# Performance work log

Measured on AMD Instinct MI355X. Metric: run time of the kernel, lower is better.

Reference implementation:

```python
import jax, jax.numpy as jnp
import numpy as np

FS = 512.0
N_PHA = 10
N_AMP = 10
FIR_LEN = 513  # odd, ~1 s at fs=512 -> resolves 2 Hz band edges
N_BINS = 18    # hard-coded in PAC.__init__
TEMP = 0.01    # ModulationIndex temperature (near-hard soft binning)
EPS = 1e-8


def _design_filters():
    # Windowed-sinc FIR bandpass, one kernel per band: h = lp(hi) - lp(lo), Hamming window.
    t = np.arange(FIR_LEN) - (FIR_LEN - 1) / 2.0
    win = np.hamming(FIR_LEN)
    def bp(lo, hi):
        lp = lambda fc: 2.0 * fc / FS * np.sinc(2.0 * fc / FS * t)
        return (lp(hi) - lp(lo)) * win
    pha_c = np.linspace(2.0, 20.0, N_PHA)
    amp_c = np.linspace(60.0, 160.0, N_AMP)
    bands = [(0.75 * c, 1.25 * c) for c in pha_c] + [(0.75 * c, 1.25 * c) for c in amp_c]
    return np.stack([bp(lo, hi) for lo, hi in bands]).astype(np.float32)  # (20, L)


def setup_inputs() -> dict:
    key = jax.random.key(0)
    x = jax.random.normal(key, (4, 16, 4096), dtype=jnp.float32)  # (B, C, T)
    filters = jnp.asarray(_design_filters())                      # (n_pha+n_amp, L)
    return {"x": x, "filters": filters}


def _analytic(sig):
    # FFT-based Hilbert analytic signal along last axis.
    T = sig.shape[-1]
    h = np.zeros(T, np.float32)
    h[0] = 1.0
    if T % 2 == 0:
        h[T // 2] = 1.0
        h[1:T // 2] = 2.0
    else:
        h[1:(T + 1) // 2] = 2.0
    return jnp.fft.ifft(jnp.fft.fft(sig, axis=-1) * jnp.asarray(h), axis=-1)


def reference(x, filters):
    B, C, T = x.shape
    L = filters.shape[-1]
    # Bandpass: (B*C, 1, T) x (n_bands, 1, L) -> (B*C, n_bands, T); symmetric kernels so corr == conv.
    xf = jax.lax.conv_general_dilated(
        x.reshape(-1, 1, T), filters[:, None, :],
        window_strides=(1,), padding=[(L // 2, L // 2)])
    xf = xf.reshape(B, C, -1, T)
    phase = jnp.angle(_analytic(xf[:, :, :N_PHA]))        # (B, C, P, T)
    amplitude = jnp.abs(_analytic(xf[:, :, N_PHA:]))      # (B, C, A, T)
    # Soft circular phase binning (temperature -> near one-hot).
    centers = jnp.asarray((-np.pi + 2.0 * np.pi * (np.arange(N_BINS) + 0.5) / N_BINS).astype(np.float32))
    d = jnp.mod(phase[..., None] - centers + np.pi, 2.0 * np.pi) - np.pi  # (B,C,P,T,K)
    w = jax.nn.softmax(-(d * d) / TEMP, axis=-1)
    # Mean amplitude per phase bin, per (pha, amp) band pair.
    amp_sum = jnp.einsum('bcptk,bcat->bcpak', w, amplitude)  # (B,C,P,A,K)
    cnt = w.sum(axis=-2)                                      # (B,C,P,K)
    mean_amp = amp_sum / (cnt[:, :, :, None, :] + EPS)
    p = mean_amp / (mean_amp.sum(-1, keepdims=True) + EPS)
    log_k = jnp.log(jnp.float32(N_BINS))
    mi = (log_k + (p * jnp.log(p + EPS)).sum(-1)) / log_k    # Tort MI, (B,C,P,A)
    return mi
```

## Files before the change

### kernel.cpp

```cpp
#include <hip/hip_runtime.h>
#include <math.h>

#define T_LEN 4096
#define FIR_L 513
#define N_PHA 10
#define N_AMP 10
#define N_BANDS 20
#define N_BINS 18
#define BC 64

typedef __attribute__((ext_vector_type(8))) short short8;
typedef __attribute__((ext_vector_type(4))) float f32x4;

#define ZA(i) (((i) << 1) + ((((i) >> 4)) << 1))

__device__ float2 twg_dev[1024];

static __device__ __forceinline__ unsigned short f2bf(float x) {
    unsigned u = __float_as_uint(x);
    unsigned r = u + 0x7FFFu + ((u >> 16) & 1u);
    return (unsigned short)(r >> 16);
}

static __device__ __forceinline__ float fast_atan2f(float y, float x) {
    const float ax = fabsf(x), ay = fabsf(y);
    const float mx = fmaxf(ax, ay), mn = fminf(ax, ay);
    const bool swap = ay > ax;
    const bool red  = mn > 0.4142135623730950f * mx;
    const float num = red ? (mn - mx) : mn;
    const float den = red ? (mn + mx) : mx;
    const float u  = num / den;
    const float z2 = u * u;
    float p = fmaf(8.05374449538e-2f, z2, -1.38776856032e-1f);
    p = fmaf(p, z2, 1.99777106478e-1f);
    p = fmaf(p, z2, -3.33329491539e-1f);
    float a = fmaf(p * z2, u, u);
    if (red)  a += 0.7853981633974483f;
    if (swap) a = 1.5707963267948966f - a;
    if (x < 0.0f) a = 3.14159265358979323f - a;
    return (y < 0.0f) ? -a : a;
}

static __device__ __forceinline__ void tw_derive(const float2* tw, int m1,
        float& c1, float& s1, float& c2, float& s2, float& c3, float& s3) {
    const float2 w1 = tw[m1];
    c1 = w1.x; s1 = w1.y;
    s2 = 2.0f * s1 * c1;
    c2 = fmaf(-2.0f * s1, s1, 1.0f);
    c3 = c1 * c2 - s1 * s2;
    s3 = s1 * c2 + c1 * s2;
}

static __device__ __forceinline__ float2 cmul_em(float2 u, float c, float s) {
    return make_float2(u.x * c + u.y * s, u.y * c - u.x * s);
}

static __device__ __forceinline__ void bf_fwd(float2& A, float2& B, float2& C, float2& D,
        float c1, float s1, float c2, float s2, float c3, float s3) {
    const float t0r = A.x + C.x, t0i = A.y + C.y;
    const float t1r = A.x - C.x, t1i = A.y - C.y;
    const float t2r = B.x + D.x, t2i = B.y + D.y;
    const float t3r = B.x - D.x, t3i = B.y - D.y;
    const float y0r = t0r + t2r,  y0i = t0i + t2i;
    const float u1r = t1r + t3i, u1i = t1i - t3r;
    const float u2r = t0r - t2r, u2i = t0i - t2i;
    const float u3r = t1r - t3i, u3i = t1i + t3r;
    A = make_float2(y0r, y0i);
    B = make_float2(u1r * c1 + u1i * s1, u1i * c1 - u1r * s1);
    C = make_float2(u2r * c2 + u2i * s2, u2i * c2 - u2r * s2);
    D = make_float2(u3r * c3 + u3i * s3, u3i * c3 - u3r * s3);
}

static __device__ __forceinline__ void bf_inv(float2& A, float2& B, float2& C, float2& D,
        float c1, float s1, float c2, float s2, float c3, float s3) {
    const float tbr = B.x * c1 - B.y * s1, tbi = B.y * c1 + B.x * s1;
    const float tcr = C.x * c2 - C.y * s2, tci = C.y * c2 + C.x * s2;
    const float tdr = D.x * c3 - D.y * s3, tdi = D.y * c3 + D.x * s3;
    const float ar = A.x, ai = A.y;
    A = make_float2(ar + tbr + tcr + tdr, ai + tbi + tci + tdi);
    B = make_float2(ar - tbi - tcr + tdi, ai + tbr - tci - tdr);
    C = make_float2(ar - tbr + tcr - tdr, ai - tbi + tci - tdi);
    D = make_float2(ar + tbi - tcr - tdi, ai - tbr - tci + tdr);
}

static __device__ __forceinline__ void fft_fwd_passes(float* z, const float2* tw,
                                                      int tid, int s0) {
    for (int s = s0; s < 6; s += 2) {
        const int hl = 10 - 2 * s;
        const int h  = 1 << hl;
        const int h4 = h >> 2;
        const int kk = tid & (h4 - 1);
        const int g  = tid >> (hl - 2);
        const int i0 = (g << (hl + 2)) + kk;
        float2 e[4][4];
#pragma unroll
        for (int j = 0; j < 4; ++j)
#pragma unroll
            for (int r = 0; r < 4; ++r)
                e[j][r] = *(const float2*)&z[ZA(i0 + j * h4 + r * h)];
#pragma unroll
        for (int j = 0; j < 4; ++j) {
            float c1, s1, c2, s2, c3, s3;
            tw_derive(tw, (kk + j * h4) << (2 * s), c1, s1, c2, s2, c3, s3);
            bf_fwd(e[j][0], e[j][1], e[j][2], e[j][3], c1, s1, c2, s2, c3, s3);
        }
        {
            float c1, s1, c2, s2, c3, s3;
            tw_derive(tw, kk << (2 * s + 2), c1, s1, c2, s2, c3, s3);
#pragma unroll
            for (int r = 0; r < 4; ++r)
                bf_fwd(e[0][r], e[1][r], e[2][r], e[3][r], c1, s1, c2, s2, c3, s3);
        }
#pragma unroll
        for (int j = 0; j < 4; ++j)
#pragma unroll
            for (int r = 0; r < 4; ++r)
                *(float2*)&z[ZA(i0 + j * h4 + r * h)] = e[j][r];
        __syncthreads();
    }
}

static __device__ __forceinline__ void fft_fwd_pass1_sparse(
        float* z, const float2* tw, int tid, float2 F, float2 Tl) {
    float c1, s1, c2, s2, c3, s3;
    tw_derive(tw, tid, c1, s1, c2, s2, c3, s3);
    float2 P[4];
    P[0] = F;
    P[1] = cmul_em(F, c1, s1);
    P[2] = cmul_em(F, c2, s2);
    P[3] = cmul_em(F, c3, s3);
    tw_derive(tw, tid + 768, c1, s1, c2, s2, c3, s3);
    const float2 iT  = make_float2(-Tl.y,  Tl.x);
    const float2 nT  = make_float2(-Tl.x, -Tl.y);
    const float2 niT = make_float2( Tl.y, -Tl.x);
    float2 Q[4];
    Q[0] = Tl;
    Q[1] = cmul_em(iT,  c1, s1);
    Q[2] = cmul_em(nT,  c2, s2);
    Q[3] = cmul_em(niT, c3, s3);
    tw_derive(tw, tid << 2, c1, s1, c2, s2, c3, s3);
#pragma unroll
    for (int r = 0; r < 4; ++r) {
        const int ib = tid + (r << 10);
        const float2 A = make_float2(P[r].x + Q[r].x, P[r].y + Q[r].y);
        const float2 B = cmul_em(make_float2(P[r].x - Q[r].y, P[r].y + Q[r].x), c1, s1);
        const float2 C = cmul_em(make_float2(P[r].x - Q[r].x, P[r].y - Q[r].y), c2, s2);
        const float2 D = cmul_em(make_float2(P[r].x + Q[r].y, P[r].y - Q[r].x), c3, s3);
        *(float2*)&z[ZA(ib)]        = A;
        *(float2*)&z[ZA(ib + 256)]  = B;
        *(float2*)&z[ZA(ib + 512)]  = C;
        *(float2*)&z[ZA(ib + 768)]  = D;
    }
}

static __device__ __forceinline__ void fft_inv6(float* z, const float2* tw, int tid) {
#pragma unroll
    for (int s = 0; s < 6; s += 2) {
        const int L  = 1 << (2 * s);
        const int k  = tid & (L - 1);
        const int g  = tid >> (2 * s);
        const int i0 = (g << (2 * s + 4)) + k;
        float2 e[4][4];
#pragma unroll
        for (int j = 0; j < 4; ++j)
#pragma unroll
            for (int r = 0; r < 4; ++r)
                e[j][r] = *(const float2*)&z[ZA(i0 + j * L + (r << (2 * s + 2)))];
        {
            float c1, s1, c2, s2, c3, s3;
            tw_derive(tw, k << (10 - 2 * s), c1, s1, c2, s2, c3, s3);
#pragma unroll
            for (int r = 0; r < 4; ++r)
                bf_inv(e[0][r], e[1][r], e[2][r], e[3][r], c1, s1, c2, s2, c3, s3);
        }
#pragma unroll
        for (int j = 0; j < 4; ++j) {
            float c1, s1, c2, s2, c3, s3;
            tw_derive(tw, (k + j * L) << (8 - 2 * s), c1, s1, c2, s2, c3, s3);
            bf_inv(e[j][0], e[j][1], e[j][2], e[j][3], c1, s1, c2, s2, c3, s3);
        }
#pragma unroll
        for (int j = 0; j < 4; ++j)
#pragma unroll
            for (int r = 0; r < 4; ++r)
                *(float2*)&z[ZA(i0 + j * L + (r << (2 * s + 2)))] = e[j][r];
        __syncthreads();
    }
}

__global__ __launch_bounds__(256) void spectral_pre(
    const float* __restrict__ x,
    const float* __restrict__ filt,
    float2* __restrict__ Xs,
    float2* __restrict__ Hs,
    float* __restrict__ corr)
{
    __shared__ __align__(16) float sm[11265];

    const int tid = threadIdx.x;
    const int b   = blockIdx.x;

    if (b == BC + N_BANDS) {
        for (int m = tid; m < 1024; m += 256) {
            float ang = (float)m * (6.283185307179586f / 4096.0f);
            float s, c;
            sincosf(ang, &s, &c);
            twg_dev[m] = make_float2(c, s);
        }
        return;
    }

    if (b > BC + N_BANDS) {
        const int cidx = b - (BC + N_BANDS + 1);
        const int bc   = cidx / N_BANDS;
        const int band = cidx % N_BANDS;
        float* xe = sm;
        float* fb = sm + 512;

        const float* xrow = x + bc * T_LEN;
        for (int i = tid; i < 512; i += 256)
            xe[i] = (i < 256) ? xrow[i] : xrow[3584 + i];
        for (int i = tid; i < FIR_L; i += 256)
            fb[i] = filt[band * FIR_L + i];
        __syncthreads();

        const int t = tid;
        float cf = 0.0f, ct = 0.0f;
        for (int l = 0; l <= 255 - t; ++l)
            cf = fmaf(fb[l], xe[256 + t + l], cf);
        for (int j = 0; j <= t; ++j)
            ct = fmaf(fb[512 - t + j], xe[j], ct);

        corr[((bc * N_BANDS + band) * 2 + 0) * 256 + t] = cf;
        corr[((bc * N_BANDS + band) * 2 + 1) * 256 + t] = ct;
        return;
    }

    float*  z   = sm;
    float2* twl = (float2*)(sm + 8704);
    float*  fb  = sm + 8704 + 2048;

    for (int m = tid; m < 1024; m += 256) {
        float ang = (float)m * (6.283185307179586f / 4096.0f);
        float s, c;
        sincosf(ang, &s, &c);
        twl[m] = make_float2(c, s);
    }

    if (b < BC) {
        const float* xrow = x + b * T_LEN;
        for (int i = tid; i < 4096; i += 256)
            *(float2*)&z[ZA(i)] = make_float2(xrow[i], 0.0f);
    } else {
        const int band = b - BC;
        for (int i = tid; i < FIR_L; i += 256) fb[i] = filt[band * FIR_L + i];
        __syncthreads();
        for (int i = tid; i < 4096; i += 256) {
            float hv = 0.0f;
            if (i < 257)        hv = fb[256 - i];
            else if (i >= 3840) hv = fb[4352 - i];
            *(float2*)&z[ZA(i)] = make_float2(hv, 0.0f);
        }
    }
    __syncthreads();

    fft_fwd_passes(z, twl, tid, 0);

    float2* dst = (b < BC) ? (Xs + b * 4096) : (Hs + (b - BC) * 4096);
    for (int i = tid; i < 4096; i += 256)
        dst[i] = *(const float2*)&z[ZA(i)];
}

__global__ __launch_bounds__(256, 4) void spectral_main_pre(
    const float* __restrict__ corr,
    const float2* __restrict__ Xs,
    const float2* __restrict__ Hs,
    float* __restrict__ pha,
    unsigned short* __restrict__ amp_bf)
{
    __shared__ __align__(16) float z[8704];

    const int tid  = threadIdx.x;
    const int bc   = blockIdx.x / N_BANDS;
    const int band = blockIdx.x % N_BANDS;
    const float2* tw = twg_dev;

    const float cf = corr[((bc * N_BANDS + band) * 2 + 0) * 256 + tid];
    const float ct = corr[((bc * N_BANDS + band) * 2 + 1) * 256 + tid];

    fft_fwd_pass1_sparse(z, tw, tid, make_float2(-cf, 0.0f), make_float2(-ct, 0.0f));
    __syncthreads();
    fft_fwd_passes(z, tw, tid, 2);

    const float2* Xrow = Xs + bc * 4096;
    const float2* Hrow = Hs + band * 4096;
#pragma unroll
    for (int k = 0; k < 8; ++k) {
        const int s = tid + (k << 8);
        const int i = ((s >> 1) << 2) | (s & 1);
        const float2 X = Xrow[i];
        const float2 H = Hrow[i];
        const float2 C = *(const float2*)&z[ZA(i)];
        const float pr = X.x * H.x - X.y * H.y + C.x;
        const float pi = X.x * H.y + X.y * H.x + C.y;
        const float mf = (i == 0) ? 1.0f : 2.0f;
        *(float2*)&z[ZA(i)] = make_float2(pr * mf, pi * mf);
    }
#pragma unroll
    for (int k = 0; k < 8; ++k) {
        const int s = tid + (k << 8);
        const int i = ((s >> 1) << 2) | 2 | (s & 1);
        if (i == 2) {
            const float2 X = Xrow[2];
            const float2 H = Hrow[2];
            const float2 C = *(const float2*)&z[ZA(2)];
            *(float2*)&z[ZA(2)] = make_float2(X.x * H.x - X.y * H.y + C.x,
                                              X.x * H.y + X.y * H.x + C.y);
        } else {
            *(float2*)&z[ZA(i)] = make_float2(0.0f, 0.0f);
        }
    }
    __syncthreads();

    fft_inv6(z, tw, tid);

    const float inv_n = 1.0f / 4096.0f;
    if (band < N_PHA) {
        float* dst = pha + (bc * N_PHA + band) * T_LEN;
        for (int i = tid; i < 4096; i += 256) {
            const float2 zz = *(const float2*)&z[ZA(i)];
            dst[i] = fast_atan2f(zz.y, zz.x);
        }
    } else {
        unsigned short* dst = amp_bf + (bc * N_AMP + (band - N_PHA)) * T_LEN;
        for (int i = tid; i < 4096; i += 256) {
            const float2 zz = *(const float2*)&z[ZA(i)];
            dst[i] = f2bf(sqrtf(zz.x * zz.x + zz.y * zz.y) * inv_n);
        }
    }
}

__global__ __launch_bounds__(256, 4) void spectral_main_inline(
    const float* __restrict__ x,
    const float* __restrict__ filt,
    const float2* __restrict__ Xs,
    const float2* __restrict__ Hs,
    float* __restrict__ pha,
    unsigned short* __restrict__ amp_bf)
{
    __shared__ float z[8704];
    __shared__ float xe[512];
    __shared__ float fb[FIR_L];

    const int tid  = threadIdx.x;
    const int bc   = blockIdx.x / N_BANDS;
    const int band = blockIdx.x % N_BANDS;
    const float2* tw = twg_dev;

    const float* xrow = x + bc * T_LEN;
    for (int i = tid; i < 512; i += 256)
        xe[i] = (i < 256) ? xrow[i] : xrow[3584 + i];
    for (int i = tid; i < FIR_L; i += 256) fb[i] = filt[band * FIR_L + i];
    __syncthreads();

    float cf = 0.0f, ct = 0.0f;
    for (int l = 0; l <= 255 - tid; ++l)
        cf = fmaf(fb[l], xe[256 + tid + l], cf);
    for (int j = 0; j <= tid; ++j)
        ct = fmaf(fb[512 - tid + j], xe[j], ct);

    fft_fwd_pass1_sparse(z, tw, tid, make_float2(-cf, 0.0f), make_float2(-ct, 0.0f));
    __syncthreads();
    fft_fwd_passes(z, tw, tid, 2);

    const float2* Xrow = Xs + bc * 4096;
    const float2* Hrow = Hs + band * 4096;
    for (int i = tid; i < 4096; i += 256) {
        const float2 X = Xrow[i];
        const float2 H = Hrow[i];
        const float2 C = *(const float2*)&z[ZA(i)];
        float pr = X.x * H.x - X.y * H.y + C.x;
        float pi = X.x * H.y + X.y * H.x + C.y;
        const int m4 = i & 3;
        const float mf = (i == 0 || i == 2) ? 1.0f : (m4 < 2 ? 2.0f : 0.0f);
        *(float2*)&z[ZA(i)] = make_float2(pr * mf, pi * mf);
    }
    __syncthreads();

    fft_inv6(z, tw, tid);

    const float inv_n = 1.0f / 4096.0f;
    if (band < N_PHA) {
        float* dst = pha + (bc * N_PHA + band) * T_LEN;
        for (int i = tid; i < 4096; i += 256) {
            const float2 zz = *(const float2*)&z[ZA(i)];
            dst[i] = fast_atan2f(zz.y, zz.x);
        }
    } else {
        unsigned short* dst = amp_bf + (bc * N_AMP + (band - N_PHA)) * T_LEN;
        for (int i = tid; i < 4096; i += 256) {
            const float2 zz = *(const float2*)&z[ZA(i)];
            dst[i] = f2bf(sqrtf(zz.x * zz.x + zz.y * zz.y) * inv_n);
        }
    }
}

__global__ __launch_bounds__(512) void bin_mi_mfma(
    const float* __restrict__ pha,
    const unsigned short* __restrict__ amp_bf,
    float* __restrict__ out)
{
    const int tid  = threadIdx.x;
    const int lane = tid & 63;
    const int wv   = tid >> 6;
    const int bc   = blockIdx.x / N_PHA;
    const int p    = blockIdx.x % N_PHA;

    __shared__ unsigned int wbufW[8][18 * 68];
    __shared__ float psum[8][11][N_BINS];
    __shared__ float asum[11][N_BINS];

    const float* phrow = pha + (bc * N_PHA + p) * T_LEN;
    const unsigned short* arow = amp_bf + bc * N_AMP * T_LEN;

    const float PI_F  = 3.14159274101257324f;
    const float INVD  = 2.8647889756541160f;
    const float DELTA = 0.34906585039886590f;
    const float C1    = 12.184696791468343f;
    const float C2    = 69.813170079773180f;

    const int m_ = lane & 15;
    const int q_ = lane >> 4;
    const int n_ = lane & 15;

    short8 zero8;
#pragma unroll
    for (int j = 0; j < 8; ++j) zero8[j] = 0;
    short8 ones8;
#pragma unroll
    for (int j = 0; j < 8; ++j) ones8[j] = (short)0x3F80;

    f32x4 acc0 = {0.f, 0.f, 0.f, 0.f};
    f32x4 acc1 = {0.f, 0.f, 0.f, 0.f};

    const int base_t = wv * 512;
    unsigned short* wh = (unsigned short*)&wbufW[wv][0];

    float2 pp[4];
#pragma unroll
    for (int c = 0; c < 4; ++c)
        pp[c] = *(const float2*)&phrow[base_t + c * 128 + lane * 2];

    for (int chunk = 0; chunk < 4; ++chunk) {
        const int cb = base_t + chunk * 128;

        short8 af[4];
#pragma unroll
        for (int s = 0; s < 4; ++s) {
            const int tA = cb + s * 32 + q_ * 8;
            if (m_ < N_AMP)       af[s] = *(const short8*)(arow + m_ * T_LEN + tA);
            else if (m_ == N_AMP) af[s] = ones8;
            else                  af[s] = zero8;
        }

#pragma unroll
        for (int k = 0; k < N_BINS; ++k)
            wbufW[wv][k * 68 + lane] = 0u;

#pragma unroll
        for (int h = 0; h < 2; ++h) {
            const float ph = h ? pp[chunk].y : pp[chunk].x;
            float u  = (ph + PI_F) * INVD;
            float jf = floorf(u);
            float d  = (u - jf - 0.5f) * DELTA;
            int j0 = (int)jf;
            if (j0 >= N_BINS) j0 -= N_BINS;
            const int jm = (j0 == 0) ? N_BINS - 1 : j0 - 1;
            const int jp = (j0 == N_BINS - 1) ? 0 : j0 + 1;
            const float em = expf(-C1 - C2 * d);
            const float ep = expf(-C1 + C2 * d);
            const float inv = 1.0f / (1.0f + em + ep);
            wh[(j0 * 68 + lane) * 2 + h] = f2bf(inv);
            wh[(jm * 68 + lane) * 2 + h] = f2bf(em * inv);
            wh[(jp * 68 + lane) * 2 + h] = f2bf(ep * inv);
        }
        __builtin_amdgcn_wave_barrier();

#pragma unroll
        for (int s = 0; s < 4; ++s) {
            const int woff = s * 16 + q_ * 4;
            short8 bfrag0 = *(const short8*)&wbufW[wv][n_ * 68 + woff];
            short8 bfrag1 = (n_ < 2)
                ? *(const short8*)&wbufW[wv][(16 + n_) * 68 + woff]
                : zero8;
            acc0 = __builtin_amdgcn_mfma_f32_16x16x32_bf16(af[s], bfrag0, acc0, 0, 0, 0);
            acc1 = __builtin_amdgcn_mfma_f32_16x16x32_bf16(af[s], bfrag1, acc1, 0, 0, 0);
        }
        __builtin_amdgcn_wave_barrier();
    }

#pragma unroll
    for (int r = 0; r < 4; ++r) {
        const int m = q_ * 4 + r;
        if (m < 11) {
            psum[wv][m][n_] = acc0[r];
            if (n_ < 2) psum[wv][m][16 + n_] = acc1[r];
        }
    }
    __syncthreads();

    if (tid < 11 * N_BINS) {
        const int m = tid / N_BINS;
        const int k = tid % N_BINS;
        float s = 0.0f;
#pragma unroll
        for (int w = 0; w < 8; ++w) s += psum[w][m][k];
        asum[m][k] = s;
    }
    __syncthreads();

    if (tid < N_AMP) {
        float ma[N_BINS];
        float msum = 0.0f;
#pragma unroll
        for (int k = 0; k < N_BINS; ++k) {
            float m = asum[tid][k] / (asum[10][k] + 1e-8f);
            ma[k] = m;
            msum += m;
        }
        const float inv = 1.0f / (msum + 1e-8f);
        float acc = 0.0f;
#pragma unroll
        for (int k = 0; k < N_BINS; ++k) {
            float pk = ma[k] * inv;
            acc = fmaf(pk, logf(pk + 1e-8f), acc);
        }
        const float logk = 2.89037175789124f;
        out[(bc * N_PHA + p) * N_AMP + tid] = (logk + acc) / logk;
    }
}

extern "C" void kernel_launch(void* const* d_in, const int* in_sizes, int n_in,
                              void* d_out, int out_size, void* d_ws, size_t ws_size,
                              hipStream_t stream) {
    const float* x    = (const float*)d_in[0];
    const float* filt = (const float*)d_in[1];
    float* out = (float*)d_out;

    float* pha = (float*)d_ws;
    unsigned short* amp_bf = (unsigned short*)(pha + BC * N_PHA * T_LEN);
    float2* Xs = (float2*)(amp_bf + BC * N_AMP * T_LEN);
    float2* Hs = Xs + BC * 4096;
    float* corr = (float*)(Hs + N_BANDS * 4096);

    const size_t need = (size_t)BC * N_PHA * T_LEN * 4
                      + (size_t)BC * N_AMP * T_LEN * 2
                      + (size_t)BC * 4096 * 8
                      + (size_t)N_BANDS * 4096 * 8
                      + (size_t)BC * N_BANDS * 2 * 256 * 4;
    const bool fits = (ws_size >= need);

    if (fits) {
        spectral_pre<<<BC + N_BANDS + 1 + BC * N_BANDS, 256, 0, stream>>>(x, filt, Xs, Hs, corr);
        spectral_main_pre<<<BC * N_BANDS, 256, 0, stream>>>(corr, Xs, Hs, pha, amp_bf);
    } else {
        spectral_pre<<<BC + N_BANDS + 1, 256, 0, stream>>>(x, filt, Xs, Hs, corr);
        spectral_main_inline<<<BC * N_BANDS, 256, 0, stream>>>(x, filt, Xs, Hs, pha, amp_bf);
    }
    bin_mi_mfma<<<BC * N_PHA, 512, 0, stream>>>(pha, amp_bf, out);
}
```

Baseline: 115.3 us.

## Fuse last forward FFT pass, spectral multiply and first inverse pass in registers

In the main spectral kernel, the final forward radix-16 pass, the Hilbert spectral multiply/mask and the first inverse radix-16 pass now run on the same 16 register-resident elements per thread. This drops two shared-memory round trips and barriers. The last inverse pass is also kept in registers, and phase and amplitude are written straight from them rather than re-read from LDS. FFT passes are split into fwd_pair/inv_pair helpers, with twiddle-free butterflies where the twiddles are trivial. The costs are higher register pressure and more complex indexing.

```diff
diff --git a/kernel.cpp b/kernel.cpp
--- a/kernel.cpp
+++ b/kernel.cpp
@@ -71,6 +71,17 @@
     D = make_float2(u3r * c3 + u3i * s3, u3i * c3 - u3r * s3);
 }
 
+static __device__ __forceinline__ void bf_fwd_nw(float2& A, float2& B, float2& C, float2& D) {
+    const float t0r = A.x + C.x, t0i = A.y + C.y;
+    const float t1r = A.x - C.x, t1i = A.y - C.y;
+    const float t2r = B.x + D.x, t2i = B.y + D.y;
+    const float t3r = B.x - D.x, t3i = B.y - D.y;
+    A = make_float2(t0r + t2r, t0i + t2i);
+    B = make_float2(t1r + t3i, t1i - t3r);
+    C = make_float2(t0r - t2r, t0i - t2i);
+    D = make_float2(t1r - t3i, t1i + t3r);
+}
+
 static __device__ __forceinline__ void bf_inv(float2& A, float2& B, float2& C, float2& D,
         float c1, float s1, float c2, float s2, float c3, float s3) {
     const float tbr = B.x * c1 - B.y * s1, tbi = B.y * c1 + B.x * s1;
@@ -83,41 +94,88 @@
     D = make_float2(ar + tbi - tcr - tdi, ai - tbr - tci + tdr);
 }
 
+static __device__ __forceinline__ void bf_inv_nw(float2& A, float2& B, float2& C, float2& D) {
+    const float tbr = B.x, tbi = B.y;
+    const float tcr = C.x, tci = C.y;
+    const float tdr = D.x, tdi = D.y;
+    const float ar = A.x, ai = A.y;
+    A = make_float2(ar + tbr + tcr + tdr, ai + tbi + tci + tdi);
+    B = make_float2(ar - tbi - tcr + tdi, ai + tbr - tci - tdr);
+    C = make_float2(ar - tbr + tcr - tdr, ai - tbi + tci - tdi);
+    D = make_float2(ar + tbi - tcr - tdi, ai - tbr - tci + tdr);
+}
+
+static __device__ __forceinline__ void fwd_pair(float* z, const float2* tw,
+                                                int tid, int s) {
+    const int hl = 10 - 2 * s;
+    const int h  = 1 << hl;
+    const int h4 = h >> 2;
+    const int kk = tid & (h4 - 1);
+    const int g  = tid >> (hl - 2);
+    const int i0 = (g << (hl + 2)) + kk;
+    float2 e[4][4];
+#pragma unroll
+    for (int j = 0; j < 4; ++j)
+#pragma unroll
+        for (int r = 0; r < 4; ++r)
+            e[j][r] = *(const float2*)&z[ZA(i0 + j * h4 + r * h)];
+#pragma unroll
+    for (int j = 0; j < 4; ++j) {
+        float c1, s1, c2, s2, c3, s3;
+        tw_derive(tw, (kk + j * h4) << (2 * s), c1, s1, c2, s2, c3, s3);
+        bf_fwd(e[j][0], e[j][1], e[j][2], e[j][3], c1, s1, c2, s2, c3, s3);
+    }
+    {
+        float c1, s1, c2, s2, c3, s3;
+        tw_derive(tw, kk << (2 * s + 2), c1, s1, c2, s2, c3, s3);
+#pragma unroll
+        for (int r = 0; r < 4; ++r)
+            bf_fwd(e[0][r], e[1][r], e[2][r], e[3][r], c1, s1, c2, s2, c3, s3);
+    }
+#pragma unroll
+    for (int j = 0; j < 4; ++j)
+#pragma unroll
+        for (int r = 0; r < 4; ++r)
+            *(float2*)&z[ZA(i0 + j * h4 + r * h)] = e[j][r];
+    __syncthreads();
+}
+
+static __device__ __forceinline__ void inv_pair(float* z, const float2* tw,
+                                                int tid, int s) {
+    const int L  = 1 << (2 * s);
+    const int k  = tid & (L - 1);
+    const int g  = tid >> (2 * s);
+    const int i0 = (g << (2 * s + 4)) + k;
+    float2 e[4][4];
+#pragma unroll
+    for (int j = 0; j < 4; ++j)
+#pragma unroll
+        for (int r = 0; r < 4; ++r)
+            e[j][r] = *(const float2*)&z[ZA(i0 + j * L + (r << (2 * s + 2)))];
+    {
+        float c1, s1, c2, s2, c3, s3;
+        tw_derive(tw, k << (10 - 2 * s), c1, s1, c2, s2, c3, s3);
+#pragma unroll
+        for (int r = 0; r < 4; ++r)
+            bf_inv(e[0][r], e[1][r], e[2][r], e[3][r], c1, s1, c2, s2, c3, s3);
+    }
+#pragma unroll
+    for (int j = 0; j < 4; ++j) {
+        float c1, s1, c2, s2, c3, s3;
+        tw_derive(tw, (k + j * L) << (8 - 2 * s), c1, s1, c2, s2, c3, s3);
+        bf_inv(e[j][0], e[j][1], e[j][2], e[j][3], c1, s1, c2, s2, c3, s3);
+    }
+#pragma unroll
+    for (int j = 0; j < 4; ++j)
+#pragma unroll
+        for (int r = 0; r < 4; ++r)
+            *(float2*)&z[ZA(i0 + j * L + (r << (2 * s + 2)))] = e[j][r];
+    __syncthreads();
+}
+
 static __device__ __forceinline__ void fft_fwd_passes(float* z, const float2* tw,
                                                       int tid, int s0) {
-    for (int s = s0; s < 6; s += 2) {
-        const int hl = 10 - 2 * s;
-        const int h  = 1 << hl;
-        const int h4 = h >> 2;
-        const int kk = tid & (h4 - 1);
-        const int g  = tid >> (hl - 2);
-        const int i0 = (g << (hl + 2)) + kk;
-        float2 e[4][4];
-#pragma unroll
-        for (int j = 0; j < 4; ++j)
-#pragma unroll
-            for (int r = 0; r < 4; ++r)
-                e[j][r] = *(const float2*)&z[ZA(i0 + j * h4 + r * h)];
-#pragma unroll
-        for (int j = 0; j < 4; ++j) {
-            float c1, s1, c2, s2, c3, s3;
-            tw_derive(tw, (kk + j * h4) << (2 * s), c1, s1, c2, s2, c3, s3);
-            bf_fwd(e[j][0], e[j][1], e[j][2], e[j][3], c1, s1, c2, s2, c3, s3);
-        }
-        {
-            float c1, s1, c2, s2, c3, s3;
-            tw_derive(tw, kk << (2 * s + 2), c1, s1, c2, s2, c3, s3);
-#pragma unroll
-            for (int r = 0; r < 4; ++r)
-                bf_fwd(e[0][r], e[1][r], e[2][r], e[3][r], c1, s1, c2, s2, c3, s3);
-        }
-#pragma unroll
-        for (int j = 0; j < 4; ++j)
-#pragma unroll
-            for (int r = 0; r < 4; ++r)
-                *(float2*)&z[ZA(i0 + j * h4 + r * h)] = e[j][r];
-        __syncthreads();
-    }
+    for (int s = s0; s < 6; s += 2) fwd_pair(z, tw, tid, s);
 }
 
 static __device__ __forceinline__ void fft_fwd_pass1_sparse(
@@ -153,41 +211,6 @@
     }
 }
 
-static __device__ __forceinline__ void fft_inv6(float* z, const float2* tw, int tid) {
-#pragma unroll
-    for (int s = 0; s < 6; s += 2) {
-        const int L  = 1 << (2 * s);
-        const int k  = tid & (L - 1);
-        const int g  = tid >> (2 * s);
-        const int i0 = (g << (2 * s + 4)) + k;
-        float2 e[4][4];
-#pragma unroll
-        for (int j = 0; j < 4; ++j)
-#pragma unroll
-            for (int r = 0; r < 4; ++r)
-                e[j][r] = *(const float2*)&z[ZA(i0 + j * L + (r << (2 * s + 2)))];
-        {
-            float c1, s1, c2, s2, c3, s3;
-            tw_derive(tw, k << (10 - 2 * s), c1, s1, c2, s2, c3, s3);
-#pragma unroll
-            for (int r = 0; r < 4; ++r)
-                bf_inv(e[0][r], e[1][r], e[2][r], e[3][r], c1, s1, c2, s2, c3, s3);
-        }
-#pragma unroll
-        for (int j = 0; j < 4; ++j) {
-            float c1, s1, c2, s2, c3, s3;
-            tw_derive(tw, (k + j * L) << (8 - 2 * s), c1, s1, c2, s2, c3, s3);
-            bf_inv(e[j][0], e[j][1], e[j][2], e[j][3], c1, s1, c2, s2, c3, s3);
-        }
-#pragma unroll
-        for (int j = 0; j < 4; ++j)
-#pragma unroll
-            for (int r = 0; r < 4; ++r)
-                *(float2*)&z[ZA(i0 + j * L + (r << (2 * s + 2)))] = e[j][r];
-        __syncthreads();
-    }
-}
-
 __global__ __launch_bounds__(256) void spectral_pre(
     const float* __restrict__ x,
     const float* __restrict__ filt,
@@ -290,53 +313,118 @@
 
     fft_fwd_pass1_sparse(z, tw, tid, make_float2(-cf, 0.0f), make_float2(-ct, 0.0f));
     __syncthreads();
-    fft_fwd_passes(z, tw, tid, 2);
-
-    const float2* Xrow = Xs + bc * 4096;
-    const float2* Hrow = Hs + band * 4096;
-#pragma unroll
-    for (int k = 0; k < 8; ++k) {
-        const int s = tid + (k << 8);
-        const int i = ((s >> 1) << 2) | (s & 1);
-        const float2 X = Xrow[i];
-        const float2 H = Hrow[i];
-        const float2 C = *(const float2*)&z[ZA(i)];
-        const float pr = X.x * H.x - X.y * H.y + C.x;
-        const float pi = X.x * H.y + X.y * H.x + C.y;
-        const float mf = (i == 0) ? 1.0f : 2.0f;
-        *(float2*)&z[ZA(i)] = make_float2(pr * mf, pi * mf);
-    }
-#pragma unroll
-    for (int k = 0; k < 8; ++k) {
-        const int s = tid + (k << 8);
-        const int i = ((s >> 1) << 2) | 2 | (s & 1);
-        if (i == 2) {
-            const float2 X = Xrow[2];
-            const float2 H = Hrow[2];
-            const float2 C = *(const float2*)&z[ZA(2)];
-            *(float2*)&z[ZA(2)] = make_float2(X.x * H.x - X.y * H.y + C.x,
-                                              X.x * H.y + X.y * H.x + C.y);
+    fwd_pair(z, tw, tid, 2);
+
+    float2 e[4][4];
+    const int base = tid << 4;
+#pragma unroll
+    for (int j = 0; j < 4; ++j)
+#pragma unroll
+        for (int r = 0; r < 4; ++r)
+            e[j][r] = *(const float2*)&z[ZA(base + j + 4 * r)];
+
+#pragma unroll
+    for (int j = 0; j < 4; ++j) {
+        if (j == 0) {
+            bf_fwd_nw(e[0][0], e[0][1], e[0][2], e[0][3]);
         } else {
-            *(float2*)&z[ZA(i)] = make_float2(0.0f, 0.0f);
-        }
-    }
-    __syncthreads();
-
-    fft_inv6(z, tw, tid);
+            float c1, s1, c2, s2, c3, s3;
+            tw_derive(tw, j << 8, c1, s1, c2, s2, c3, s3);
+            bf_fwd(e[j][0], e[j][1], e[j][2], e[j][3], c1, s1, c2, s2, c3, s3);
+        }
+    }
+#pragma unroll
+    for (int r = 0; r < 4; ++r)
+        bf_fwd_nw(e[0][r], e[1][r], e[2][r], e[3][r]);
+
+    {
+        const float2* Xrow = Xs + bc * 4096;
+        const float2* Hrow = Hs + band * 4096;
+#pragma unroll
+        for (int r = 0; r < 4; ++r) {
+            const int i2 = base + 4 * r;
+            const float4 Xp = *(const float4*)&Xrow[i2];
+            const float4 Hp = *(const float4*)&Hrow[i2];
+            {
+                const float pr = Xp.x * Hp.x - Xp.y * Hp.y + e[0][r].x;
+                const float pi = Xp.x * Hp.y + Xp.y * Hp.x + e[0][r].y;
+                const float mf = (i2 == 0) ? 1.0f : 2.0f;
+                e[0][r] = make_float2(pr * mf, pi * mf);
+            }
+            {
+                const float pr = Xp.z * Hp.z - Xp.w * Hp.w + e[1][r].x;
+                const float pi = Xp.z * Hp.w + Xp.w * Hp.z + e[1][r].y;
+                e[1][r] = make_float2(pr * 2.0f, pi * 2.0f);
+            }
+            if (i2 == 0) {
+                const float2 X2 = Xrow[2];
+                const float2 H2 = Hrow[2];
+                e[2][r] = make_float2(X2.x * H2.x - X2.y * H2.y + e[2][r].x,
+                                      X2.x * H2.y + X2.y * H2.x + e[2][r].y);
+            } else {
+                e[2][r] = make_float2(0.0f, 0.0f);
+            }
+            e[3][r] = make_float2(0.0f, 0.0f);
+        }
+    }
+
+#pragma unroll
+    for (int r = 0; r < 4; ++r)
+        bf_inv_nw(e[0][r], e[1][r], e[2][r], e[3][r]);
+#pragma unroll
+    for (int j = 0; j < 4; ++j) {
+        if (j == 0) {
+            bf_inv_nw(e[0][0], e[0][1], e[0][2], e[0][3]);
+        } else {
+            float c1, s1, c2, s2, c3, s3;
+            tw_derive(tw, j << 8, c1, s1, c2, s2, c3, s3);
+            bf_inv(e[j][0], e[j][1], e[j][2], e[j][3], c1, s1, c2, s2, c3, s3);
+        }
+    }
+#pragma unroll
+    for (int j = 0; j < 4; ++j)
+#pragma unroll
+        for (int r = 0; r < 4; ++r)
+            *(float2*)&z[ZA(base + j + 4 * r)] = e[j][r];
+    __syncthreads();
+
+    inv_pair(z, tw, tid, 2);
+
+#pragma unroll
+    for (int j = 0; j < 4; ++j)
+#pragma unroll
+        for (int r = 0; r < 4; ++r)
+            e[j][r] = *(const float2*)&z[ZA(tid + (j << 8) + (r << 10))];
+    {
+        float c1, s1, c2, s2, c3, s3;
+        tw_derive(tw, tid << 2, c1, s1, c2, s2, c3, s3);
+#pragma unroll
+        for (int r = 0; r < 4; ++r)
+            bf_inv(e[0][r], e[1][r], e[2][r], e[3][r], c1, s1, c2, s2, c3, s3);
+    }
+#pragma unroll
+    for (int j = 0; j < 4; ++j) {
+        float c1, s1, c2, s2, c3, s3;
+        tw_derive(tw, tid + (j << 8), c1, s1, c2, s2, c3, s3);
+        bf_inv(e[j][0], e[j][1], e[j][2], e[j][3], c1, s1, c2, s2, c3, s3);
+    }
 
     const float inv_n = 1.0f / 4096.0f;
     if (band < N_PHA) {
         float* dst = pha + (bc * N_PHA + band) * T_LEN;
-        for (int i = tid; i < 4096; i += 256) {
-            const float2 zz = *(const float2*)&z[ZA(i)];
-            dst[i] = fast_atan2f(zz.y, zz.x);
-        }
+#pragma unroll
+        for (int j = 0; j < 4; ++j)
+#pragma unroll
+            for (int r = 0; r < 4; ++r)
+                dst[tid + (j << 8) + (r << 10)] = fast_atan2f(e[j][r].y, e[j][r].x);
     } else {
         unsigned short* dst = amp_bf + (bc * N_AMP + (band - N_PHA)) * T_LEN;
-        for (int i = tid; i < 4096; i += 256) {
-            const float2 zz = *(const float2*)&z[ZA(i)];
-            dst[i] = f2bf(sqrtf(zz.x * zz.x + zz.y * zz.y) * inv_n);
-        }
+#pragma unroll
+        for (int j = 0; j < 4; ++j)
+#pragma unroll
+            for (int r = 0; r < 4; ++r)
+                dst[tid + (j << 8) + (r << 10)] =
+                    f2bf(sqrtf(e[j][r].x * e[j][r].x + e[j][r].y * e[j][r].y) * inv_n);
     }
 }
 
@@ -371,7 +459,8 @@
 
     fft_fwd_pass1_sparse(z, tw, tid, make_float2(-cf, 0.0f), make_float2(-ct, 0.0f));
     __syncthreads();
-    fft_fwd_passes(z, tw, tid, 2);
+    fwd_pair(z, tw, tid, 2);
+    fwd_pair(z, tw, tid, 4);
 
     const float2* Xrow = Xs + bc * 4096;
     const float2* Hrow = Hs + band * 4096;
@@ -387,7 +476,9 @@
     }
     __syncthreads();
 
-    fft_inv6(z, tw, tid);
+    inv_pair(z, tw, tid, 0);
+    inv_pair(z, tw, tid, 2);
+    inv_pair(z, tw, tid, 4);
 
     const float inv_n = 1.0f / 4096.0f;
     if (band < N_PHA) {
```

Result: slower. 119.2 us (+3.3%).
